# Performance work log

Measured on AMD Instinct MI355X. Metric: run time of the kernel, lower is better.

## Reference

```python
import jax, jax.numpy as jnp
import numpy as np

B, N, D, O = 128, 256, 512, 512
EPS = 1e-5


def setup_inputs() -> dict:
    key = jax.random.key(0)
    ks = jax.random.split(key, 12)
    Observation = jax.random.normal(ks[0], (B, N, D), dtype=jnp.float32)
    mask = jax.random.bernoulli(ks[1], 0.7, (B, N))
    s = 0.02
    W1 = jax.random.normal(ks[2], (D, O), dtype=jnp.float32) * s
    W2 = jax.random.normal(ks[3], (O, O), dtype=jnp.float32) * s
    W3 = jax.random.normal(ks[4], (O, O), dtype=jnp.float32) * s
    g1 = 1.0 + 0.1 * jax.random.normal(ks[5], (D,), dtype=jnp.float32)
    b1 = 0.02 * jax.random.normal(ks[6], (D,), dtype=jnp.float32)
    g2 = 1.0 + 0.1 * jax.random.normal(ks[7], (O,), dtype=jnp.float32)
    b2 = 0.02 * jax.random.normal(ks[8], (O,), dtype=jnp.float32)
    g3 = 1.0 + 0.1 * jax.random.normal(ks[9], (O,), dtype=jnp.float32)
    b3 = 0.02 * jax.random.normal(ks[10], (O,), dtype=jnp.float32)
    return {"Observation": Observation, "mask": mask,
            "g1": g1, "b1": b1, "W1": W1,
            "g2": g2, "b2": b2, "W2": W2,
            "g3": g3, "b3": b3, "W3": W3}


def layer_norm(x, g, b):
    m = jnp.mean(x, axis=-1, keepdims=True)
    v = jnp.mean(jnp.square(x - m), axis=-1, keepdims=True)
    return (x - m) * jax.lax.rsqrt(v + EPS) * g + b


def reference(Observation, mask, g1, b1, W1, g2, b2, W2, g3, b3, W3):
    Bv, Nv, Dv = Observation.shape
    # _grant_at_least_one_valid: force element 0 valid if a row is all-invalid
    all_invalid = ~jnp.any(mask, axis=1)  # [B]
    mask = mask | (all_invalid[:, None] & (jnp.arange(Nv) == 0)[None, :])
    x = Observation.reshape(-1, Dv)  # [B*N, D]
    # Block 1: LN -> Linear (no bias) -> Tanh (dropout is eval identity)
    h1 = jnp.tanh(layer_norm(x, g1, b1) @ W1)
    # Block 2
    h2 = jnp.tanh(layer_norm(h1, g2, b2) @ W2)
    # Block 3 with residual input (h2 + h1), no activation
    o3 = layer_norm(h2 + h1, g3, b3) @ W3  # [B*N, O]
    fill = jnp.finfo(o3.dtype).min
    o3 = jnp.where(mask.reshape(-1, 1), o3, fill)
    out = jax.nn.softmax(o3.reshape(Bv, Nv, -1), axis=1)
    return jnp.nan_to_num(out, nan=0.0)
```

## Files before the change

kernel.cpp:

```cpp
#include <hip/hip_runtime.h>


#define RTOT 32768
#define NN   256

typedef _Float16 f16;
typedef __attribute__((ext_vector_type(4))) _Float16 f16x4;
typedef __attribute__((ext_vector_type(8))) _Float16 f16x8;
typedef __attribute__((ext_vector_type(4))) float f32x4;

#define EPS16 520
#define EPS32 516

__device__ __forceinline__ float fast_tanh(float x) {
  float e = __expf(2.f * x);
  return 1.f - 2.f * __builtin_amdgcn_rcpf(e + 1.f);
}
__device__ __forceinline__ void async_copy16(const void* g, void* l) {
  __builtin_amdgcn_global_load_lds(
      (const __attribute__((address_space(1))) unsigned int*)g,
      (__attribute__((address_space(3))) unsigned int*)l, 16, 0, 0);
}

__global__ void prep_w_kernel(const float* __restrict__ W1, const float* __restrict__ W2,
                              const float* __restrict__ W3, f16* __restrict__ WT) {
  int idx = blockIdx.x * 256 + threadIdx.x;
  int s   = idx >> 18;
  int rem = idx & 0x3FFFF;
  int o   = rem >> 9;
  int d   = rem & 511;
  const float* W = (s == 0) ? W1 : (s == 1) ? W2 : W3;
  WT[idx] = (f16)W[d * 512 + o];
}

__global__ __launch_bounds__(256) void ln1_kernel(const float* __restrict__ in,
                                                  const float* __restrict__ g,
                                                  const float* __restrict__ b,
                                                  f16* __restrict__ outA) {
  int wv = threadIdx.x >> 6, lane = threadIdx.x & 63;
  size_t row = (size_t)blockIdx.x * 4 + wv;
  const float* x = in + (row << 9);
  float4 v0 = *(const float4*)(x + lane * 4);
  float4 v1 = *(const float4*)(x + 256 + lane * 4);
  float s = v0.x + v0.y + v0.z + v0.w + v1.x + v1.y + v1.z + v1.w;
  float q = v0.x*v0.x + v0.y*v0.y + v0.z*v0.z + v0.w*v0.w
          + v1.x*v1.x + v1.y*v1.y + v1.z*v1.z + v1.w*v1.w;
  #pragma unroll
  for (int off = 1; off < 64; off <<= 1) {
    s += __shfl_xor(s, off, 64);
    q += __shfl_xor(q, off, 64);
  }
  float mean = s * (1.f / 512.f);
  float var  = q * (1.f / 512.f) - mean * mean;
  float inv  = 1.f / sqrtf(var + 1e-5f);
  float4 g0 = *(const float4*)(g + lane * 4);
  float4 b0 = *(const float4*)(b + lane * 4);
  float4 g1 = *(const float4*)(g + 256 + lane * 4);
  float4 b1 = *(const float4*)(b + 256 + lane * 4);
  f16x4 o0, o1;
  o0[0] = (f16)((v0.x - mean) * inv * g0.x + b0.x);
  o0[1] = (f16)((v0.y - mean) * inv * g0.y + b0.y);
  o0[2] = (f16)((v0.z - mean) * inv * g0.z + b0.z);
  o0[3] = (f16)((v0.w - mean) * inv * g0.w + b0.w);
  o1[0] = (f16)((v1.x - mean) * inv * g1.x + b1.x);
  o1[1] = (f16)((v1.y - mean) * inv * g1.y + b1.y);
  o1[2] = (f16)((v1.z - mean) * inv * g1.z + b1.z);
  o1[3] = (f16)((v1.w - mean) * inv * g1.w + b1.w);
  *(f16x4*)&outA[(row << 9) + lane * 4] = o0;
  *(f16x4*)&outA[(row << 9) + 256 + lane * 4] = o1;
}

template <int STAGE>
__global__ __launch_bounds__(512, 4) void fused_kernel(
    const f16* __restrict__ A, const f16* __restrict__ BT,
    const float* __restrict__ g, const float* __restrict__ b,
    f16* __restrict__ H1, f16* __restrict__ outH, float* __restrict__ outF) {
  __shared__ __align__(16) char smem[73728];
  __shared__ __align__(16) float2 sPart[512];
  __shared__ __align__(16) float2 sStat[64];
  f16* sA = (f16*)smem;
  f16* sB = (f16*)(smem + 8192);

  int t = threadIdx.x, lane = t & 63, wv = t >> 6;
  int row16 = lane & 15, quad = lane >> 4;
  int rBase = blockIdx.x * 64;
  int lr  = lane >> 3;
  int lcs = ((lane & 7) ^ (lane >> 3)) * 8;

  f32x4 acc[4][4] = {};

  for (int k0 = 0; k0 < 512; k0 += 64) {
    {
      const f16* ga = A + (((size_t)(rBase + wv * 8 + lr)) << 9) + k0 + lcs;
      async_copy16(ga, sA + (wv * 8) * 64);
    }
    #pragma unroll
    for (int p = 0; p < 8; ++p) {
      int r = wv * 64 + p * 8;
      const f16* gb = BT + (((size_t)(r + lr)) << 9) + k0 + lcs;
      async_copy16(gb, sB + r * 64);
    }
    __syncthreads();
    #pragma unroll
    for (int kk = 0; kk < 64; kk += 32) {
      int kb = kk >> 3;
      f16x8 af[4], bf[4];
      #pragma unroll
      for (int i = 0; i < 4; ++i) {
        int ar = i * 16 + row16;
        int br = wv * 64 + i * 16 + row16;
        af[i] = *(const f16x8*)&sA[ar * 64 + (((quad + kb) ^ (ar & 7)) << 3)];
        bf[i] = *(const f16x8*)&sB[br * 64 + (((quad + kb) ^ (br & 7)) << 3)];
      }
      #pragma unroll
      for (int mi = 0; mi < 4; ++mi)
        #pragma unroll
        for (int ni = 0; ni < 4; ++ni)
          acc[mi][ni] = __builtin_amdgcn_mfma_f32_16x16x32_f16(af[mi], bf[ni], acc[mi][ni], 0, 0, 0);
    }
    __syncthreads();
  }

  if constexpr (STAGE == 2) {
    float* sE = (float*)smem;
    #pragma unroll
    for (int half = 0; half < 2; ++half) {
      #pragma unroll
      for (int mi = 0; mi < 2; ++mi) {
        int rt = half * 2 + mi;
        #pragma unroll
        for (int ni = 0; ni < 4; ++ni) {
          int col = wv * 64 + ni * 16 + row16;
          #pragma unroll
          for (int rg = 0; rg < 4; ++rg)
            sE[(mi * 16 + quad * 4 + rg) * EPS32 + col] = acc[rt][ni][rg];
        }
      }
      __syncthreads();
      #pragma unroll
      for (int i = 0; i < 8; ++i) {
        int gi = t + i * 512;
        int row = gi >> 7, cg = (gi & 127) * 4;
        f32x4 v = *(const f32x4*)&sE[row * EPS32 + cg];
        *(f32x4*)&outF[(((size_t)(rBase + half * 32 + row)) << 9) + cg] = v;
      }
      __syncthreads();
    }
    return;
  } else {
    float gv[4], bv[4];
    #pragma unroll
    for (int ni = 0; ni < 4; ++ni) {
      int c = wv * 64 + ni * 16 + row16;
      gv[ni] = g[c]; bv[ni] = b[c];
    }

    f16* sH = (f16*)smem;
    if constexpr (STAGE == 1) {
      #pragma unroll
      for (int p = 0; p < 8; ++p) {
        const f16* gh = H1 + (((size_t)(rBase + wv * 8 + p)) << 9) + lane * 8;
        async_copy16(gh, sH + (wv * 8 + p) * 512);
      }
    }

    #pragma unroll
    for (int mi = 0; mi < 4; ++mi)
      #pragma unroll
      for (int ni = 0; ni < 4; ++ni)
        #pragma unroll
        for (int rg = 0; rg < 4; ++rg)
          acc[mi][ni][rg] = fast_tanh(acc[mi][ni][rg]);

    if constexpr (STAGE == 1) {
      __syncthreads();
      #pragma unroll
      for (int mi = 0; mi < 4; ++mi)
        #pragma unroll
        for (int ni = 0; ni < 4; ++ni) {
          int col = wv * 64 + ni * 16 + row16;
          #pragma unroll
          for (int rg = 0; rg < 4; ++rg)
            acc[mi][ni][rg] += (float)sH[(mi * 16 + quad * 4 + rg) * 512 + col];
        }
    }

    f16* sE = (f16*)smem;
    if constexpr (STAGE == 0) {
      #pragma unroll
      for (int mi = 0; mi < 4; ++mi)
        #pragma unroll
        for (int ni = 0; ni < 4; ++ni) {
          int col = wv * 64 + ni * 16 + row16;
          #pragma unroll
          for (int rg = 0; rg < 4; ++rg)
            sE[(mi * 16 + quad * 4 + rg) * EPS16 + col] = (f16)acc[mi][ni][rg];
        }
    }

    #pragma unroll
    for (int mi = 0; mi < 4; ++mi)
      #pragma unroll
      for (int rg = 0; rg < 4; ++rg) {
        float s = 0.f, q = 0.f;
        #pragma unroll
        for (int ni = 0; ni < 4; ++ni) {
          float v = acc[mi][ni][rg];
          s += v; q += v * v;
        }
        #pragma unroll
        for (int off = 1; off < 16; off <<= 1) {
          s += __shfl_xor(s, off, 16);
          q += __shfl_xor(q, off, 16);
        }
        if (row16 == 0)
          sPart[wv * 64 + mi * 16 + quad * 4 + rg] = make_float2(s, q);
      }
    __syncthreads();

    if (t < 64) {
      float s = 0.f, q = 0.f;
      #pragma unroll
      for (int w = 0; w < 8; ++w) {
        float2 p = sPart[w * 64 + t];
        s += p.x; q += p.y;
      }
      float mean = s * (1.f / 512.f);
      float var  = q * (1.f / 512.f) - mean * mean;
      sStat[t] = make_float2(mean, 1.f / sqrtf(var + 1e-5f));
    }
    if constexpr (STAGE == 0) {
      #pragma unroll
      for (int i = 0; i < 8; ++i) {
        int gi = t + i * 512;
        int row = gi >> 6, cg = (gi & 63) * 8;
        f16x8 v = *(const f16x8*)&sE[row * EPS16 + cg];
        *(f16x8*)&H1[(((size_t)(rBase + row)) << 9) + cg] = v;
      }
    }
    __syncthreads();

    #pragma unroll
    for (int mi = 0; mi < 4; ++mi)
      #pragma unroll
      for (int rg = 0; rg < 4; ++rg) {
        int row = mi * 16 + quad * 4 + rg;
        float2 st = sStat[row];
        #pragma unroll
        for (int ni = 0; ni < 4; ++ni) {
          int col = wv * 64 + ni * 16 + row16;
          sE[row * EPS16 + col] = (f16)((acc[mi][ni][rg] - st.x) * st.y * gv[ni] + bv[ni]);
        }
      }
    __syncthreads();

    #pragma unroll
    for (int i = 0; i < 8; ++i) {
      int gi = t + i * 512;
      int row = gi >> 6, cg = (gi & 63) * 8;
      f16x8 v = *(const f16x8*)&sE[row * EPS16 + cg];
      *(f16x8*)&outH[(((size_t)(rBase + row)) << 9) + cg] = v;
    }
  }
}

__global__ __launch_bounds__(256, 2) void softmax_kernel(const float* __restrict__ o3,
                                                         const int* __restrict__ mask,
                                                         float* __restrict__ out) {
  __shared__ float sz[NN * 64];
  __shared__ float sredm[4 * 64];
  __shared__ float sreds[4 * 64];
  __shared__ int   smask[NN];

  int b  = blockIdx.x >> 3;
  int oc = blockIdx.x & 7;
  int t  = threadIdx.x;
  int o_l = t & 63;
  int n_h = t >> 6;

  int mt = mask[b * NN + t];
  int any = __syncthreads_or(mt);
  smask[t] = (t == 0 && !any) ? 1 : mt;
  __syncthreads();

  const float* src = o3 + (((size_t)(b * NN)) << 9) + oc * 64;
  #pragma unroll 4
  for (int j = 0; j < 64; ++j) {
    int n = j * 4 + n_h;
    float v = src[((size_t)n << 9) + o_l];
    sz[n * 64 + o_l] = smask[n] ? v : -3.4e38f;
  }
  __syncthreads();

  float mx = -3.4e38f;
  #pragma unroll 8
  for (int i = 0; i < 64; ++i)
    mx = fmaxf(mx, sz[(n_h * 64 + i) * 64 + o_l]);
  sredm[n_h * 64 + o_l] = mx;
  __syncthreads();
  float m4 = fmaxf(fmaxf(sredm[o_l], sredm[64 + o_l]),
                   fmaxf(sredm[128 + o_l], sredm[192 + o_l]));

  float sm = 0.f;
  #pragma unroll 8
  for (int i = 0; i < 64; ++i)
    sm += __expf(sz[(n_h * 64 + i) * 64 + o_l] - m4);
  sreds[n_h * 64 + o_l] = sm;
  __syncthreads();
  float tot = sreds[o_l] + sreds[64 + o_l] + sreds[128 + o_l] + sreds[192 + o_l];
  float inv = 1.f / tot;

  float* dst = out + (((size_t)(b * NN)) << 9) + oc * 64;
  #pragma unroll 4
  for (int j = 0; j < 64; ++j) {
    int n = j * 4 + n_h;
    dst[((size_t)n << 9) + o_l] = __expf(sz[n * 64 + o_l] - m4) * inv;
  }
}

extern "C" void kernel_launch(void* const* d_in, const int* in_sizes, int n_in,
                              void* d_out, int out_size, void* d_ws, size_t ws_size,
                              hipStream_t stream) {
  const float* Obs = (const float*)d_in[0];
  const int*   msk = (const int*)d_in[1];
  const float* g1  = (const float*)d_in[2];
  const float* b1  = (const float*)d_in[3];
  const float* W1  = (const float*)d_in[4];
  const float* g2  = (const float*)d_in[5];
  const float* b2  = (const float*)d_in[6];
  const float* W2  = (const float*)d_in[7];
  const float* g3  = (const float*)d_in[8];
  const float* b3  = (const float*)d_in[9];
  const float* W3  = (const float*)d_in[10];
  float* out = (float*)d_out;

  char* ws = (char*)d_ws;
  const size_t MB = 1u << 20;
  f16*   Ah0 = (f16*)ws;
  f16*   Ah1 = (f16*)(ws + 32 * MB);
  f16*   H1h = (f16*)(ws + 64 * MB);
  float* Lg  = (float*)(ws + 64 * MB);
  f16*   WT  = (f16*)(ws + 128 * MB);

  prep_w_kernel<<<3072, 256, 0, stream>>>(W1, W2, W3, WT);
  ln1_kernel<<<8192, 256, 0, stream>>>(Obs, g1, b1, Ah0);
  fused_kernel<0><<<512, 512, 0, stream>>>(Ah0, WT,          g2, b2, H1h, Ah1, nullptr);
  fused_kernel<1><<<512, 512, 0, stream>>>(Ah1, WT + 262144, g3, b3, H1h, Ah0, nullptr);
  fused_kernel<2><<<512, 512, 0, stream>>>(Ah0, WT + 524288, nullptr, nullptr, nullptr, nullptr, Lg);
  softmax_kernel<<<1024, 256, 0, stream>>>(Lg, msk, out);
}
```

Baseline: 305.4 us.

## Fuse LN1 and three GEMM stages into one kernel keeping activations in LDS

Replaces the separate LN1 kernel and three per-stage fused GEMM kernels with one mega-kernel. Each block computes LN1 for its 64 rows into shared memory, then chains the three matmuls, keeping the LN-normalised activations in LDS and h1 in registers. This removes the global round trips for the intermediate f16 activations and h1, plus three kernel launches. Weight tiles are streamed through double-buffered 32-wide K chunks. The larger shared-memory footprint (about 134 KB) and higher register use may lower occupancy, and the weights are re-read per block for every stage.

```diff
diff --git a/kernel.cpp b/kernel.cpp
--- a/kernel.cpp
+++ b/kernel.cpp
@@ -1,15 +1,14 @@
 #include <hip/hip_runtime.h>
 
 
-#define RTOT 32768
-#define NN   256
+#define NN 256
 
 typedef _Float16 f16;
 typedef __attribute__((ext_vector_type(4))) _Float16 f16x4;
 typedef __attribute__((ext_vector_type(8))) _Float16 f16x8;
 typedef __attribute__((ext_vector_type(4))) float f32x4;
 
-#define EPS16 520
+#define XS    520
 #define EPS32 516
 
 __device__ __forceinline__ float fast_tanh(float x) {
@@ -33,233 +32,217 @@
   WT[idx] = (f16)W[d * 512 + o];
 }
 
-__global__ __launch_bounds__(256) void ln1_kernel(const float* __restrict__ in,
-                                                  const float* __restrict__ g,
-                                                  const float* __restrict__ b,
-                                                  f16* __restrict__ outA) {
-  int wv = threadIdx.x >> 6, lane = threadIdx.x & 63;
-  size_t row = (size_t)blockIdx.x * 4 + wv;
-  const float* x = in + (row << 9);
-  float4 v0 = *(const float4*)(x + lane * 4);
-  float4 v1 = *(const float4*)(x + 256 + lane * 4);
-  float s = v0.x + v0.y + v0.z + v0.w + v1.x + v1.y + v1.z + v1.w;
-  float q = v0.x*v0.x + v0.y*v0.y + v0.z*v0.z + v0.w*v0.w
-          + v1.x*v1.x + v1.y*v1.y + v1.z*v1.z + v1.w*v1.w;
+__device__ __forceinline__ void stage_b(const f16* __restrict__ Bg, f16* __restrict__ dst,
+                                        int wv, int lane, int c) {
   #pragma unroll
-  for (int off = 1; off < 64; off <<= 1) {
-    s += __shfl_xor(s, off, 64);
-    q += __shfl_xor(q, off, 64);
-  }
-  float mean = s * (1.f / 512.f);
-  float var  = q * (1.f / 512.f) - mean * mean;
-  float inv  = 1.f / sqrtf(var + 1e-5f);
-  float4 g0 = *(const float4*)(g + lane * 4);
-  float4 b0 = *(const float4*)(b + lane * 4);
-  float4 g1 = *(const float4*)(g + 256 + lane * 4);
-  float4 b1 = *(const float4*)(b + 256 + lane * 4);
-  f16x4 o0, o1;
-  o0[0] = (f16)((v0.x - mean) * inv * g0.x + b0.x);
-  o0[1] = (f16)((v0.y - mean) * inv * g0.y + b0.y);
-  o0[2] = (f16)((v0.z - mean) * inv * g0.z + b0.z);
-  o0[3] = (f16)((v0.w - mean) * inv * g0.w + b0.w);
-  o1[0] = (f16)((v1.x - mean) * inv * g1.x + b1.x);
-  o1[1] = (f16)((v1.y - mean) * inv * g1.y + b1.y);
-  o1[2] = (f16)((v1.z - mean) * inv * g1.z + b1.z);
-  o1[3] = (f16)((v1.w - mean) * inv * g1.w + b1.w);
-  *(f16x4*)&outA[(row << 9) + lane * 4] = o0;
-  *(f16x4*)&outA[(row << 9) + 256 + lane * 4] = o1;
-}
-
-template <int STAGE>
-__global__ __launch_bounds__(512, 4) void fused_kernel(
-    const f16* __restrict__ A, const f16* __restrict__ BT,
-    const float* __restrict__ g, const float* __restrict__ b,
-    f16* __restrict__ H1, f16* __restrict__ outH, float* __restrict__ outF) {
-  __shared__ __align__(16) char smem[73728];
-  __shared__ __align__(16) float2 sPart[512];
-  __shared__ __align__(16) float2 sStat[64];
-  f16* sA = (f16*)smem;
-  f16* sB = (f16*)(smem + 8192);
+  for (int q = 0; q < 4; ++q) {
+    int r0 = wv * 64 + q * 16;
+    const f16* gb = Bg + (((size_t)(r0 + (lane >> 2))) << 9) + c * 32 + (lane & 3) * 8;
+    async_copy16(gb, dst + r0 * 32);
+  }
+}
+
+__global__ __launch_bounds__(512, 2) void mega_kernel(
+    const float* __restrict__ Obs,
+    const float* __restrict__ g1, const float* __restrict__ b1,
+    const f16* __restrict__ WT,
+    const float* __restrict__ g2, const float* __restrict__ b2,
+    const float* __restrict__ g3, const float* __restrict__ b3,
+    float* __restrict__ outF) {
+  __shared__ __align__(16) char smem[136704];
+  f16* sX  = (f16*)smem;
+  f16* sB0 = (f16*)(smem + 66560);
+  f16* sB1 = (f16*)(smem + 99328);
+  float2* sPart = (float2*)(smem + 132096);
+  float2* sStat = (float2*)(smem + 136192);
 
   int t = threadIdx.x, lane = t & 63, wv = t >> 6;
   int row16 = lane & 15, quad = lane >> 4;
   int rBase = blockIdx.x * 64;
-  int lr  = lane >> 3;
-  int lcs = ((lane & 7) ^ (lane >> 3)) * 8;
-
-  f32x4 acc[4][4] = {};
-
-  for (int k0 = 0; k0 < 512; k0 += 64) {
-    {
-      const f16* ga = A + (((size_t)(rBase + wv * 8 + lr)) << 9) + k0 + lcs;
-      async_copy16(ga, sA + (wv * 8) * 64);
-    }
+
+  stage_b(WT, sB0, wv, lane, 0);
+
+  {
+    float4 w0 = *(const float4*)(g1 + lane * 4);
+    float4 u0 = *(const float4*)(b1 + lane * 4);
+    float4 w1 = *(const float4*)(g1 + 256 + lane * 4);
+    float4 u1 = *(const float4*)(b1 + 256 + lane * 4);
     #pragma unroll
     for (int p = 0; p < 8; ++p) {
-      int r = wv * 64 + p * 8;
-      const f16* gb = BT + (((size_t)(r + lr)) << 9) + k0 + lcs;
-      async_copy16(gb, sB + r * 64);
+      int row = wv * 8 + p;
+      const float* x = Obs + (((size_t)(rBase + row)) << 9);
+      float4 v0 = *(const float4*)(x + lane * 4);
+      float4 v1 = *(const float4*)(x + 256 + lane * 4);
+      float s = v0.x + v0.y + v0.z + v0.w + v1.x + v1.y + v1.z + v1.w;
+      float q = v0.x*v0.x + v0.y*v0.y + v0.z*v0.z + v0.w*v0.w
+              + v1.x*v1.x + v1.y*v1.y + v1.z*v1.z + v1.w*v1.w;
+      #pragma unroll
+      for (int off = 1; off < 64; off <<= 1) {
+        s += __shfl_xor(s, off, 64);
+        q += __shfl_xor(q, off, 64);
+      }
+      float mean = s * (1.f / 512.f);
+      float var  = q * (1.f / 512.f) - mean * mean;
+      float inv  = 1.f / sqrtf(var + 1e-5f);
+      f16x4 o0, o1;
+      o0[0] = (f16)((v0.x - mean) * inv * w0.x + u0.x);
+      o0[1] = (f16)((v0.y - mean) * inv * w0.y + u0.y);
+      o0[2] = (f16)((v0.z - mean) * inv * w0.z + u0.z);
+      o0[3] = (f16)((v0.w - mean) * inv * w0.w + u0.w);
+      o1[0] = (f16)((v1.x - mean) * inv * w1.x + u1.x);
+      o1[1] = (f16)((v1.y - mean) * inv * w1.y + u1.y);
+      o1[2] = (f16)((v1.z - mean) * inv * w1.z + u1.z);
+      o1[3] = (f16)((v1.w - mean) * inv * w1.w + u1.w);
+      *(f16x4*)&sX[row * XS + lane * 4] = o0;
+      *(f16x4*)&sX[row * XS + 256 + lane * 4] = o1;
     }
-    __syncthreads();
+  }
+
+  f32x4 acc[4][4];
+  f16x4 h1s[4][4];
+
+  __syncthreads();
+
+  for (int g = 0; g < 3; ++g) {
+    const f16* Bg = WT + ((size_t)g << 18);
+
     #pragma unroll
-    for (int kk = 0; kk < 64; kk += 32) {
-      int kb = kk >> 3;
+    for (int mi = 0; mi < 4; ++mi)
+      #pragma unroll
+      for (int ni = 0; ni < 4; ++ni)
+        acc[mi][ni] = (f32x4){0.f, 0.f, 0.f, 0.f};
+
+    for (int c = 0; c < 16; ++c) {
+      if (c < 15) stage_b(Bg, (c & 1) ? sB0 : sB1, wv, lane, c + 1);
+
+      const f16* bb = (c & 1) ? sB1 : sB0;
       f16x8 af[4], bf[4];
       #pragma unroll
       for (int i = 0; i < 4; ++i) {
         int ar = i * 16 + row16;
+        af[i] = *(const f16x8*)&sX[ar * XS + c * 32 + quad * 8];
         int br = wv * 64 + i * 16 + row16;
-        af[i] = *(const f16x8*)&sA[ar * 64 + (((quad + kb) ^ (ar & 7)) << 3)];
-        bf[i] = *(const f16x8*)&sB[br * 64 + (((quad + kb) ^ (br & 7)) << 3)];
+        bf[i] = *(const f16x8*)&bb[br * 32 + quad * 8];
       }
       #pragma unroll
       for (int mi = 0; mi < 4; ++mi)
         #pragma unroll
         for (int ni = 0; ni < 4; ++ni)
           acc[mi][ni] = __builtin_amdgcn_mfma_f32_16x16x32_f16(af[mi], bf[ni], acc[mi][ni], 0, 0, 0);
-    }
-    __syncthreads();
-  }
-
-  if constexpr (STAGE == 2) {
-    float* sE = (float*)smem;
-    #pragma unroll
-    for (int half = 0; half < 2; ++half) {
-      #pragma unroll
-      for (int mi = 0; mi < 2; ++mi) {
-        int rt = half * 2 + mi;
-        #pragma unroll
-        for (int ni = 0; ni < 4; ++ni) {
-          int col = wv * 64 + ni * 16 + row16;
-          #pragma unroll
-          for (int rg = 0; rg < 4; ++rg)
-            sE[(mi * 16 + quad * 4 + rg) * EPS32 + col] = acc[rt][ni][rg];
-        }
-      }
-      __syncthreads();
-      #pragma unroll
-      for (int i = 0; i < 8; ++i) {
-        int gi = t + i * 512;
-        int row = gi >> 7, cg = (gi & 127) * 4;
-        f32x4 v = *(const f32x4*)&sE[row * EPS32 + cg];
-        *(f32x4*)&outF[(((size_t)(rBase + half * 32 + row)) << 9) + cg] = v;
-      }
+
       __syncthreads();
     }
-    return;
-  } else {
-    float gv[4], bv[4];
-    #pragma unroll
-    for (int ni = 0; ni < 4; ++ni) {
-      int c = wv * 64 + ni * 16 + row16;
-      gv[ni] = g[c]; bv[ni] = b[c];
-    }
-
-    f16* sH = (f16*)smem;
-    if constexpr (STAGE == 1) {
-      #pragma unroll
-      for (int p = 0; p < 8; ++p) {
-        const f16* gh = H1 + (((size_t)(rBase + wv * 8 + p)) << 9) + lane * 8;
-        async_copy16(gh, sH + (wv * 8 + p) * 512);
-      }
-    }
-
-    #pragma unroll
-    for (int mi = 0; mi < 4; ++mi)
-      #pragma unroll
-      for (int ni = 0; ni < 4; ++ni)
-        #pragma unroll
-        for (int rg = 0; rg < 4; ++rg)
-          acc[mi][ni][rg] = fast_tanh(acc[mi][ni][rg]);
-
-    if constexpr (STAGE == 1) {
+
+    if (g == 2) {
+      float* sE = (float*)smem;
+      #pragma unroll
+      for (int half = 0; half < 2; ++half) {
+        #pragma unroll
+        for (int mi = 0; mi < 2; ++mi) {
+          int rt = half * 2 + mi;
+          #pragma unroll
+          for (int ni = 0; ni < 4; ++ni) {
+            int col = wv * 64 + ni * 16 + row16;
+            #pragma unroll
+            for (int rg = 0; rg < 4; ++rg)
+              sE[(mi * 16 + quad * 4 + rg) * EPS32 + col] = acc[rt][ni][rg];
+          }
+        }
+        __syncthreads();
+        #pragma unroll
+        for (int i = 0; i < 8; ++i) {
+          int gi = t + i * 512;
+          int row = gi >> 7, cg = (gi & 127) * 4;
+          f32x4 v = *(const f32x4*)&sE[row * EPS32 + cg];
+          *(f32x4*)&outF[(((size_t)(rBase + half * 32 + row)) << 9) + cg] = v;
+        }
+        __syncthreads();
+      }
+    } else {
+      #pragma unroll
+      for (int mi = 0; mi < 4; ++mi)
+        #pragma unroll
+        for (int ni = 0; ni < 4; ++ni)
+          #pragma unroll
+          for (int rg = 0; rg < 4; ++rg)
+            acc[mi][ni][rg] = fast_tanh(acc[mi][ni][rg]);
+
+      if (g == 0) {
+        #pragma unroll
+        for (int mi = 0; mi < 4; ++mi)
+          #pragma unroll
+          for (int ni = 0; ni < 4; ++ni) {
+            f16x4 h;
+            #pragma unroll
+            for (int rg = 0; rg < 4; ++rg) h[rg] = (f16)acc[mi][ni][rg];
+            h1s[mi][ni] = h;
+          }
+      } else {
+        #pragma unroll
+        for (int mi = 0; mi < 4; ++mi)
+          #pragma unroll
+          for (int ni = 0; ni < 4; ++ni)
+            #pragma unroll
+            for (int rg = 0; rg < 4; ++rg)
+              acc[mi][ni][rg] += (float)h1s[mi][ni][rg];
+      }
+
+      stage_b(WT + ((size_t)(g + 1) << 18), sB0, wv, lane, 0);
+
+      const float* gp = (g == 0) ? g2 : g3;
+      const float* bp = (g == 0) ? b2 : b3;
+      float gva[4], bva[4];
+      #pragma unroll
+      for (int ni = 0; ni < 4; ++ni) {
+        int col = wv * 64 + ni * 16 + row16;
+        gva[ni] = gp[col]; bva[ni] = bp[col];
+      }
+
+      #pragma unroll
+      for (int mi = 0; mi < 4; ++mi)
+        #pragma unroll
+        for (int rg = 0; rg < 4; ++rg) {
+          float s = 0.f, q = 0.f;
+          #pragma unroll
+          for (int ni = 0; ni < 4; ++ni) {
+            float v = acc[mi][ni][rg];
+            s += v; q += v * v;
+          }
+          #pragma unroll
+          for (int off = 1; off < 16; off <<= 1) {
+            s += __shfl_xor(s, off, 16);
+            q += __shfl_xor(q, off, 16);
+          }
+          if (row16 == 0)
+            sPart[wv * 64 + mi * 16 + quad * 4 + rg] = make_float2(s, q);
+        }
       __syncthreads();
+      if (t < 64) {
+        float s = 0.f, q = 0.f;
+        #pragma unroll
+        for (int w = 0; w < 8; ++w) {
+          float2 p = sPart[w * 64 + t];
+          s += p.x; q += p.y;
+        }
+        float mean = s * (1.f / 512.f);
+        float var  = q * (1.f / 512.f) - mean * mean;
+        sStat[t] = make_float2(mean, 1.f / sqrtf(var + 1e-5f));
+      }
+      __syncthreads();
+
       #pragma unroll
       for (int mi = 0; mi < 4; ++mi)
         #pragma unroll
-        for (int ni = 0; ni < 4; ++ni) {
-          int col = wv * 64 + ni * 16 + row16;
-          #pragma unroll
-          for (int rg = 0; rg < 4; ++rg)
-            acc[mi][ni][rg] += (float)sH[(mi * 16 + quad * 4 + rg) * 512 + col];
-        }
-    }
-
-    f16* sE = (f16*)smem;
-    if constexpr (STAGE == 0) {
-      #pragma unroll
-      for (int mi = 0; mi < 4; ++mi)
-        #pragma unroll
-        for (int ni = 0; ni < 4; ++ni) {
-          int col = wv * 64 + ni * 16 + row16;
-          #pragma unroll
-          for (int rg = 0; rg < 4; ++rg)
-            sE[(mi * 16 + quad * 4 + rg) * EPS16 + col] = (f16)acc[mi][ni][rg];
-        }
-    }
-
-    #pragma unroll
-    for (int mi = 0; mi < 4; ++mi)
-      #pragma unroll
-      for (int rg = 0; rg < 4; ++rg) {
-        float s = 0.f, q = 0.f;
-        #pragma unroll
-        for (int ni = 0; ni < 4; ++ni) {
-          float v = acc[mi][ni][rg];
-          s += v; q += v * v;
-        }
-        #pragma unroll
-        for (int off = 1; off < 16; off <<= 1) {
-          s += __shfl_xor(s, off, 16);
-          q += __shfl_xor(q, off, 16);
-        }
-        if (row16 == 0)
-          sPart[wv * 64 + mi * 16 + quad * 4 + rg] = make_float2(s, q);
-      }
-    __syncthreads();
-
-    if (t < 64) {
-      float s = 0.f, q = 0.f;
-      #pragma unroll
-      for (int w = 0; w < 8; ++w) {
-        float2 p = sPart[w * 64 + t];
-        s += p.x; q += p.y;
-      }
-      float mean = s * (1.f / 512.f);
-      float var  = q * (1.f / 512.f) - mean * mean;
-      sStat[t] = make_float2(mean, 1.f / sqrtf(var + 1e-5f));
-    }
-    if constexpr (STAGE == 0) {
-      #pragma unroll
-      for (int i = 0; i < 8; ++i) {
-        int gi = t + i * 512;
-        int row = gi >> 6, cg = (gi & 63) * 8;
-        f16x8 v = *(const f16x8*)&sE[row * EPS16 + cg];
-        *(f16x8*)&H1[(((size_t)(rBase + row)) << 9) + cg] = v;
-      }
-    }
-    __syncthreads();
-
-    #pragma unroll
-    for (int mi = 0; mi < 4; ++mi)
-      #pragma unroll
-      for (int rg = 0; rg < 4; ++rg) {
-        int row = mi * 16 + quad * 4 + rg;
-        float2 st = sStat[row];
-        #pragma unroll
-        for (int ni = 0; ni < 4; ++ni) {
-          int col = wv * 64 + ni * 16 + row16;
-          sE[row * EPS16 + col] = (f16)((acc[mi][ni][rg] - st.x) * st.y * gv[ni] + bv[ni]);
-        }
-      }
-    __syncthreads();
-
-    #pragma unroll
-    for (int i = 0; i < 8; ++i) {
-      int gi = t + i * 512;
-      int row = gi >> 6, cg = (gi & 63) * 8;
-      f16x8 v = *(const f16x8*)&sE[row * EPS16 + cg];
-      *(f16x8*)&outH[(((size_t)(rBase + row)) << 9) + cg] = v;
+        for (int rg = 0; rg < 4; ++rg) {
+          int row = mi * 16 + quad * 4 + rg;
+          float2 st = sStat[row];
+          #pragma unroll
+          for (int ni = 0; ni < 4; ++ni) {
+            int col = wv * 64 + ni * 16 + row16;
+            sX[row * XS + col] = (f16)((acc[mi][ni][rg] - st.x) * st.y * gva[ni] + bva[ni]);
+          }
+        }
+      __syncthreads();
     }
   }
 }
@@ -336,16 +319,10 @@
 
   char* ws = (char*)d_ws;
   const size_t MB = 1u << 20;
-  f16*   Ah0 = (f16*)ws;
-  f16*   Ah1 = (f16*)(ws + 32 * MB);
-  f16*   H1h = (f16*)(ws + 64 * MB);
-  float* Lg  = (float*)(ws + 64 * MB);
-  f16*   WT  = (f16*)(ws + 128 * MB);
+  float* Lg = (float*)ws;
+  f16*   WT = (f16*)(ws + 64 * MB);
 
   prep_w_kernel<<<3072, 256, 0, stream>>>(W1, W2, W3, WT);
-  ln1_kernel<<<8192, 256, 0, stream>>>(Obs, g1, b1, Ah0);
-  fused_kernel<0><<<512, 512, 0, stream>>>(Ah0, WT,          g2, b2, H1h, Ah1, nullptr);
-  fused_kernel<1><<<512, 512, 0, stream>>>(Ah1, WT + 262144, g3, b3, H1h, Ah0, nullptr);
-  fused_kernel<2><<<512, 512, 0, stream>>>(Ah0, WT + 524288, nullptr, nullptr, nullptr, nullptr, Lg);
+  mega_kernel<<<512, 512, 0, stream>>>(Obs, g1, b1, WT, g2, b2, g3, b3, Lg);
   softmax_kernel<<<1024, 256, 0, stream>>>(Lg, msk, out);
 }
```

Measured after the change: 325.4 us. 6.5% more time.
